# Performance work log

Hardware: AMD Instinct MI355X
Metric: run time of the kernel (lower is better)

The kernel has to match this reference:

```python
import jax, jax.numpy as jnp
import numpy as np
from math import factorial, sqrt

RS_IN = [(64, 0, 0), (64, 1, 0), (32, 2, 0)]
BATCH = 256


def _w3j(j1, j2, j3, m1, m2, m3):
    # Racah formula for the Wigner 3j symbol (integer l's)
    if m1 + m2 + m3 != 0 or not (abs(j1 - j2) <= j3 <= j1 + j2):
        return 0.0
    if abs(m1) > j1 or abs(m2) > j2 or abs(m3) > j3:
        return 0.0
    f = factorial
    pref = (-1.0) ** (j1 - j2 - m3) * sqrt(
        f(j1 + j2 - j3) * f(j1 - j2 + j3) * f(-j1 + j2 + j3) / f(j1 + j2 + j3 + 1)
        * f(j1 + m1) * f(j1 - m1) * f(j2 + m2) * f(j2 - m2) * f(j3 + m3) * f(j3 - m3))
    kmin = max(0, j2 - j3 - m1, j1 - j3 + m2)
    kmax = min(j1 + j2 - j3, j1 - m1, j2 + m2)
    s = 0.0
    for k in range(kmin, kmax + 1):
        s += (-1.0) ** k / (f(k) * f(j1 + j2 - j3 - k) * f(j1 - m1 - k)
                            * f(j2 + m2 - k) * f(j3 - j2 + m1 + k) * f(j3 - j1 - m2 + k))
    return pref * s


def _q(l):
    # unitary change of basis: complex spherical harmonics -> real basis
    q = np.zeros((2 * l + 1, 2 * l + 1), dtype=complex)
    q[l, l] = 1.0
    for m in range(1, l + 1):
        q[l + m, l + m] = (-1) ** m / sqrt(2)
        q[l + m, l - m] = 1 / sqrt(2)
        q[l - m, l - m] = 1j / sqrt(2)
        q[l - m, l + m] = -1j * (-1) ** m / sqrt(2)
    return q


def _real_w3j(la, lb, lc):
    # real-basis Wigner 3j tensor of shape (2la+1, 2lb+1, 2lc+1), Frobenius norm 1
    Cc = np.zeros((2 * la + 1, 2 * lb + 1, 2 * lc + 1))
    for ma in range(-la, la + 1):
        for mb in range(-lb, lb + 1):
            mc = -(ma + mb)
            if abs(mc) <= lc:
                Cc[la + ma, lb + mb, lc + mc] = _w3j(la, lb, lc, ma, mb, mc)
    T = np.einsum('im,jn,ko,mno->ijk', _q(la), _q(lb), _q(lc), Cc.astype(complex))
    idx = np.argmax(np.abs(T))
    T = T / (T.flat[idx] / abs(T.flat[idx]))  # fix global phase -> real tensor
    assert np.abs(T.imag).max() < 1e-6
    return np.real(T)


def _simplify(Rs):
    out = []
    for mul, l, p in Rs:
        if out and out[-1][1:] == (l, p):
            out[-1] = (out[-1][0] + mul, l, p)
        elif mul > 0:
            out.append((mul, l, p))
    return out


def _build(Rs_in):
    # Replicates e3nn tensor_square(Rs_in, sorted=True) with 'component' normalization,
    # producing the sparse mixing matrix as (row, col_i, col_j, value) with
    # col = col_i * dim_in + col_j  (never materialized densely).
    Rs = _simplify(Rs_in)
    dim_in = sum(m * (2 * l + 1) for m, l, _ in Rs)
    rows, ci, cj, vals, Rs_out = [], [], [], [], []
    index_out = 0
    index_1 = 0
    for a, (mul1, l1, p1) in enumerate(Rs):
        dim1 = mul1 * (2 * l1 + 1)
        # diagonal block: irrep with itself (sym/antisym multiplicity pairs)
        for lo in range(0, 2 * l1 + 1):
            w_all = np.arange(mul1 * mul1)
            u, v = w_all // mul1, w_all % mul1
            mask = (u <= v) if lo % 2 == 0 else (u < v)
            u, v = u[mask], v[mask]
            cnt = u.size
            if cnt == 0:
                continue
            C = _real_w3j(lo, l1, l1) * sqrt(2 * lo + 1)  # component norm
            k, i1, i2 = np.nonzero(C)
            cv = C[k, i1, i2]
            w = np.arange(cnt)
            rows.append((w[:, None] * (2 * lo + 1) + k[None, :]).ravel() + index_out)
            ci.append((u[:, None] * (2 * l1 + 1) + i1[None, :]).ravel() + index_1)
            cj.append((v[:, None] * (2 * l1 + 1) + i2[None, :]).ravel() + index_1)
            vals.append(np.tile(cv, cnt))
            Rs_out.append((cnt, lo, p1 * p1))
            index_out += cnt * (2 * lo + 1)
        index_2 = index_1 + dim1
        # off-diagonal blocks
        for (mul2, l2, p2) in Rs[a + 1:]:
            dim2 = mul2 * (2 * l2 + 1)
            for lo in range(abs(l1 - l2), l1 + l2 + 1):
                C = _real_w3j(lo, l1, l2) * sqrt(2 * lo + 1)
                k, i1, i2 = np.nonzero(C)
                cv = C[k, i1, i2]
                cnt = mul1 * mul2
                w = np.arange(cnt)
                u, v = w // mul2, w % mul2
                rows.append((w[:, None] * (2 * lo + 1) + k[None, :]).ravel() + index_out)
                ci.append((u[:, None] * (2 * l1 + 1) + i1[None, :]).ravel() + index_1)
                cj.append((v[:, None] * (2 * l2 + 1) + i2[None, :]).ravel() + index_2)
                vals.append(np.tile(cv, cnt))
                Rs_out.append((cnt, lo, p1 * p2))
                index_out += cnt * (2 * lo + 1)
            index_2 += dim2
        index_1 += dim1
    Rs_out = _simplify(Rs_out)
    # stable sort of output irreps by (l, p) -> row permutation (sorted=True)
    xs, j = [], 0
    for mul, l, p in Rs_out:
        d = mul * (2 * l + 1)
        xs.append((l, p, mul, j, d))
        j += d
    old2new = np.empty(j, dtype=np.int64)
    i = 0
    for l, p, mul, jj, d in sorted(xs):
        old2new[jj:jj + d] = np.arange(i, i + d)
        i += d
    rows = old2new[np.concatenate(rows)]
    return (rows.astype(np.int32), np.concatenate(ci).astype(np.int32),
            np.concatenate(cj).astype(np.int32),
            np.concatenate(vals).astype(np.float32), int(i), int(dim_in))


_ROWS, _COLI, _COLJ, _VALS, _DIM_OUT, _DIM_IN = _build(RS_IN)


def setup_inputs() -> dict:
    key = jax.random.key(0)
    features = jax.random.normal(key, (BATCH, _DIM_IN), dtype=jnp.float32)
    return {
        'features': features,
        'vals': jnp.asarray(_VALS),
        'rows': jnp.asarray(_ROWS),
        'col_i': jnp.asarray(_COLI),
        'col_j': jnp.asarray(_COLJ),
        'dim_out': _DIM_OUT,
    }


def reference(features, vals, rows, col_i, col_j, dim_out):
    # out[z, r] = sum_e vals[e] * f[z, col_i[e]] * f[z, col_j[e]]  scattered into rows[e]
    f = features.reshape(-1, features.shape[-1])              # (Z, dim_in)
    contrib = vals[None, :] * f[:, col_i] * f[:, col_j]       # (Z, nnz)
    out = jax.ops.segment_sum(contrib.T, rows, num_segments=dim_out)  # (dim_out, Z)
    return out.T.reshape(*features.shape[:-1], -1)
```

## Files before the change

### kernel.cpp

```cpp
#include <hip/hip_runtime.h>

#define BATCH 256
#define ZTILE 16
#define NZT 2
#define PADF 20
#define DIN_CAP 416

__global__ __launch_bounds__(256) void prep_t(
    const float* __restrict__ f, const int* __restrict__ rows,
    int* __restrict__ rstart, int* __restrict__ rend,
    float* __restrict__ fT, int nnz, int dim_in, int TB, int ctiles)
{
    const int bx = blockIdx.x;
    if (bx < TB) {
        __shared__ float lt[32][33];
        const int c0 = (bx % ctiles) * 32;
        const int z0 = (bx / ctiles) * 32;
        const int ic = threadIdx.x & 31;
        const int i0 = threadIdx.x >> 5;
#pragma unroll
        for (int k = 0; k < 4; ++k) {
            const int a = i0 + 8 * k;
            const int c = c0 + ic;
            lt[a][ic] = (c < dim_in) ? f[(size_t)(z0 + a) * dim_in + c] : 0.0f;
        }
        __syncthreads();
#pragma unroll
        for (int k = 0; k < 4; ++k) {
            const int b = i0 + 8 * k;
            const int c = c0 + b;
            if (c < dim_in)
                fT[(size_t)c * BATCH + z0 + ic] = lt[ic][b];
        }
    } else {
        const int e = (bx - TB) * 256 + threadIdx.x;
        if (e < nnz) {
            const int r = rows[e];
            if (e == 0 || rows[e - 1] != r) rstart[r] = e;
            if (e == nnz - 1 || rows[e + 1] != r) rend[r] = e + 1;
        }
    }
}

__device__ __forceinline__ void lds_sync()
{
    asm volatile("s_waitcnt lgkmcnt(0)" ::: "memory");
    __builtin_amdgcn_sched_barrier(0);
    __builtin_amdgcn_s_barrier();
    __builtin_amdgcn_sched_barrier(0);
}

__global__ __launch_bounds__(256) void tsq_main(
    const float* __restrict__ fT, const float* __restrict__ vals,
    const int* __restrict__ ci, const int* __restrict__ cj,
    const int* __restrict__ rstart, const int* __restrict__ rend,
    float* __restrict__ out, int dim_in, int dim_out, int nnz)
{
    __shared__ __align__(16) float fzT[DIN_CAP * PADF];

    const int r = blockIdx.x * blockDim.x + threadIdx.x;
    const bool valid = (r < dim_out);

    int s = 0, e1 = 0;
    if (valid) {
        const int ss = rstart[r];
        const int ee = rend[r];
        if (ss >= 0 && ee > ss && ee <= nnz) { s = ss; e1 = ee; }
    }

    const int zbase = blockIdx.y * (ZTILE * NZT);
    const int nchunk = dim_in * (ZTILE / 4);

    for (int t = 0; t < NZT; ++t) {
        const int z0 = zbase + t * ZTILE;

        for (int i = threadIdx.x; i < nchunk; i += blockDim.x) {
            const int c  = i >> 2;
            const int zq = i & 3;
            const float4 v = *(const float4*)(fT + (size_t)c * BATCH + z0 + zq * 4);
            *(float4*)(fzT + c * PADF + zq * 4) = v;
        }
        lds_sync();

        float4 a0 = {0,0,0,0}, a1 = {0,0,0,0}, a2 = {0,0,0,0}, a3 = {0,0,0,0};
        for (int e = s; e < e1; ++e) {
            const int   a = ci[e];
            const int   b = cj[e];
            const float v = vals[e];
            const float* ba = fzT + a * PADF;
            const float* bb = fzT + b * PADF;
            float4 xa, xb;
            xa = *(const float4*)(ba);      xb = *(const float4*)(bb);
            a0.x += v*xa.x*xb.x; a0.y += v*xa.y*xb.y; a0.z += v*xa.z*xb.z; a0.w += v*xa.w*xb.w;
            xa = *(const float4*)(ba + 4);  xb = *(const float4*)(bb + 4);
            a1.x += v*xa.x*xb.x; a1.y += v*xa.y*xb.y; a1.z += v*xa.z*xb.z; a1.w += v*xa.w*xb.w;
            xa = *(const float4*)(ba + 8);  xb = *(const float4*)(bb + 8);
            a2.x += v*xa.x*xb.x; a2.y += v*xa.y*xb.y; a2.z += v*xa.z*xb.z; a2.w += v*xa.w*xb.w;
            xa = *(const float4*)(ba + 12); xb = *(const float4*)(bb + 12);
            a3.x += v*xa.x*xb.x; a3.y += v*xa.y*xb.y; a3.z += v*xa.z*xb.z; a3.w += v*xa.w*xb.w;
        }

        if (valid) {
            float* o = out + (size_t)z0 * dim_out + r;
            const size_t d = dim_out;
            __builtin_nontemporal_store(a0.x, o);          __builtin_nontemporal_store(a0.y, o + d);
            __builtin_nontemporal_store(a0.z, o + 2*d);    __builtin_nontemporal_store(a0.w, o + 3*d);
            __builtin_nontemporal_store(a1.x, o + 4*d);    __builtin_nontemporal_store(a1.y, o + 5*d);
            __builtin_nontemporal_store(a1.z, o + 6*d);    __builtin_nontemporal_store(a1.w, o + 7*d);
            __builtin_nontemporal_store(a2.x, o + 8*d);    __builtin_nontemporal_store(a2.y, o + 9*d);
            __builtin_nontemporal_store(a2.z, o + 10*d);   __builtin_nontemporal_store(a2.w, o + 11*d);
            __builtin_nontemporal_store(a3.x, o + 12*d);   __builtin_nontemporal_store(a3.y, o + 13*d);
            __builtin_nontemporal_store(a3.z, o + 14*d);   __builtin_nontemporal_store(a3.w, o + 15*d);
        }
        lds_sync();
    }
}

__global__ __launch_bounds__(256) void tsq_fallback(
    const float* __restrict__ f, const float* __restrict__ vals,
    const int* __restrict__ ci, const int* __restrict__ cj,
    const int* __restrict__ rstart, const int* __restrict__ rend,
    float* __restrict__ out, int dim_in, int dim_out, int nnz)
{
    const int r = blockIdx.x * blockDim.x + threadIdx.x;
    if (r >= dim_out) return;
    const int z = blockIdx.y;
    const float* __restrict__ fb = f + (size_t)z * dim_in;
    const int ss = rstart[r];
    const int ee = rend[r];
    float acc = 0.0f;
    if (ss >= 0 && ee > ss && ee <= nnz) {
        for (int e = ss; e < ee; ++e)
            acc += vals[e] * fb[ci[e]] * fb[cj[e]];
    }
    out[(size_t)z * dim_out + r] = acc;
}

extern "C" void kernel_launch(void* const* d_in, const int* in_sizes, int n_in,
                              void* d_out, int out_size, void* d_ws, size_t ws_size,
                              hipStream_t stream)
{
    const float* f    = (const float*)d_in[0];
    const float* vals = (const float*)d_in[1];
    const int*   rows = (const int*)d_in[2];
    const int*   ci   = (const int*)d_in[3];
    const int*   cj   = (const int*)d_in[4];
    float*       out  = (float*)d_out;

    const int nnz     = in_sizes[1];
    const int nF      = in_sizes[0];
    const int dim_in  = nF / BATCH;
    const int dim_out = out_size / BATCH;

    int*   rstart = (int*)d_ws;
    int*   rend   = rstart + dim_out;
    float* fT     = (float*)(rend + dim_out);

    const int use_main = (dim_in <= DIN_CAP) &&
                         (ws_size >= (size_t)(2 * dim_out) * 4 + (size_t)nF * 4);

    const int ctiles = (dim_in + 31) / 32;
    const int TB = use_main ? ctiles * (BATCH / 32) : 0;
    const int NB = (nnz + 255) / 256;
    prep_t<<<TB + NB, 256, 0, stream>>>(f, rows, rstart, rend, fT,
                                        nnz, dim_in, TB, ctiles);

    if (use_main) {
        dim3 grid((dim_out + 255) / 256, BATCH / (ZTILE * NZT));
        tsq_main<<<grid, 256, 0, stream>>>(fT, vals, ci, cj, rstart, rend, out,
                                           dim_in, dim_out, nnz);
    } else {
        dim3 grid((dim_out + 255) / 256, BATCH);
        tsq_fallback<<<grid, 256, 0, stream>>>(f, vals, ci, cj, rstart, rend,
                                               out, dim_in, dim_out, nnz);
    }
}
```

Baseline: 35.79 us.

## Map output rows to waves with lanes over batch, staging output through LDS

Replaces the thread-per-row kernel that staged batch tiles of transposed features in LDS with a kernel where each wave handles eight output rows and each lane covers four batch entries, reading feature rows straight from the transposed global buffer. The results are collected in an LDS tile and then written out as row-coalesced stores. This removes the per-tile LDS fill and the barriers, and it removes divergence from rows with different nonzero counts, because all lanes in a wave share the same nonzero loop. The cost is that per-row work is serialized within a wave and feature reads now come from global memory or cache instead of LDS.

```diff
diff --git a/kernel.cpp b/kernel.cpp
--- a/kernel.cpp
+++ b/kernel.cpp
@@ -1,10 +1,11 @@
 #include <hip/hip_runtime.h>
 
 #define BATCH 256
-#define ZTILE 16
-#define NZT 2
-#define PADF 20
-#define DIN_CAP 416
+#define RPB 32
+#define RPW 8
+#define LSTR 260
+
+typedef float __attribute__((ext_vector_type(4))) fx4;
 
 __global__ __launch_bounds__(256) void prep_t(
     const float* __restrict__ f, const int* __restrict__ rows,
@@ -42,77 +43,56 @@
     }
 }
 
-__device__ __forceinline__ void lds_sync()
-{
-    asm volatile("s_waitcnt lgkmcnt(0)" ::: "memory");
-    __builtin_amdgcn_sched_barrier(0);
-    __builtin_amdgcn_s_barrier();
-    __builtin_amdgcn_sched_barrier(0);
-}
-
-__global__ __launch_bounds__(256) void tsq_main(
+__global__ __launch_bounds__(256) void tsq_rowwave(
     const float* __restrict__ fT, const float* __restrict__ vals,
     const int* __restrict__ ci, const int* __restrict__ cj,
     const int* __restrict__ rstart, const int* __restrict__ rend,
-    float* __restrict__ out, int dim_in, int dim_out, int nnz)
+    float* __restrict__ out, int dim_out, int nnz)
 {
-    __shared__ __align__(16) float fzT[DIN_CAP * PADF];
+    __shared__ __align__(16) float ot[RPB][LSTR];
 
-    const int r = blockIdx.x * blockDim.x + threadIdx.x;
-    const bool valid = (r < dim_out);
+    const int lane = threadIdx.x & 63;
+    const int wave = threadIdx.x >> 6;
+    const int r0   = blockIdx.x * RPB;
 
-    int s = 0, e1 = 0;
-    if (valid) {
-        const int ss = rstart[r];
-        const int ee = rend[r];
-        if (ss >= 0 && ee > ss && ee <= nnz) { s = ss; e1 = ee; }
+    for (int i = 0; i < RPW; ++i) {
+        const int rl = wave * RPW + i;
+        const int r  = r0 + rl;
+        fx4 acc = {0.f, 0.f, 0.f, 0.f};
+        if (r < dim_out) {
+            const int ss = rstart[r];
+            const int ee = rend[r];
+            if (ss >= 0 && ee > ss && ee <= nnz) {
+                for (int e = ss; e < ee; ++e) {
+                    const int   a = ci[e];
+                    const int   b = cj[e];
+                    const float v = vals[e];
+                    const fx4 xa = *(const fx4*)(fT + (size_t)a * BATCH + 4 * lane);
+                    const fx4 xb = *(const fx4*)(fT + (size_t)b * BATCH + 4 * lane);
+                    acc += v * xa * xb;
+                }
+            }
+        }
+        *(fx4*)(&ot[rl][4 * lane]) = acc;
     }
+    __syncthreads();
 
-    const int zbase = blockIdx.y * (ZTILE * NZT);
-    const int nchunk = dim_in * (ZTILE / 4);
-
-    for (int t = 0; t < NZT; ++t) {
-        const int z0 = zbase + t * ZTILE;
-
-        for (int i = threadIdx.x; i < nchunk; i += blockDim.x) {
-            const int c  = i >> 2;
-            const int zq = i & 3;
-            const float4 v = *(const float4*)(fT + (size_t)c * BATCH + z0 + zq * 4);
-            *(float4*)(fzT + c * PADF + zq * 4) = v;
+    const int rl   = threadIdx.x & 31;
+    const int qsel = threadIdx.x >> 5;
+    const int r    = r0 + rl;
+    if (r < dim_out) {
+        const size_t d = dim_out;
+#pragma unroll
+        for (int k = 0; k < 8; ++k) {
+            const int q = qsel + 8 * k;
+            const fx4 v = *(const fx4*)(&ot[rl][4 * q]);
+            const int z = 4 * q;
+            float* o = out + (size_t)z * d + r;
+            __builtin_nontemporal_store(v.x, o);
+            __builtin_nontemporal_store(v.y, o + d);
+            __builtin_nontemporal_store(v.z, o + 2 * d);
+            __builtin_nontemporal_store(v.w, o + 3 * d);
         }
-        lds_sync();
-
-        float4 a0 = {0,0,0,0}, a1 = {0,0,0,0}, a2 = {0,0,0,0}, a3 = {0,0,0,0};
-        for (int e = s; e < e1; ++e) {
-            const int   a = ci[e];
-            const int   b = cj[e];
-            const float v = vals[e];
-            const float* ba = fzT + a * PADF;
-            const float* bb = fzT + b * PADF;
-            float4 xa, xb;
-            xa = *(const float4*)(ba);      xb = *(const float4*)(bb);
-            a0.x += v*xa.x*xb.x; a0.y += v*xa.y*xb.y; a0.z += v*xa.z*xb.z; a0.w += v*xa.w*xb.w;
-            xa = *(const float4*)(ba + 4);  xb = *(const float4*)(bb + 4);
-            a1.x += v*xa.x*xb.x; a1.y += v*xa.y*xb.y; a1.z += v*xa.z*xb.z; a1.w += v*xa.w*xb.w;
-            xa = *(const float4*)(ba + 8);  xb = *(const float4*)(bb + 8);
-            a2.x += v*xa.x*xb.x; a2.y += v*xa.y*xb.y; a2.z += v*xa.z*xb.z; a2.w += v*xa.w*xb.w;
-            xa = *(const float4*)(ba + 12); xb = *(const float4*)(bb + 12);
-            a3.x += v*xa.x*xb.x; a3.y += v*xa.y*xb.y; a3.z += v*xa.z*xb.z; a3.w += v*xa.w*xb.w;
-        }
-
-        if (valid) {
-            float* o = out + (size_t)z0 * dim_out + r;
-            const size_t d = dim_out;
-            __builtin_nontemporal_store(a0.x, o);          __builtin_nontemporal_store(a0.y, o + d);
-            __builtin_nontemporal_store(a0.z, o + 2*d);    __builtin_nontemporal_store(a0.w, o + 3*d);
-            __builtin_nontemporal_store(a1.x, o + 4*d);    __builtin_nontemporal_store(a1.y, o + 5*d);
-            __builtin_nontemporal_store(a1.z, o + 6*d);    __builtin_nontemporal_store(a1.w, o + 7*d);
-            __builtin_nontemporal_store(a2.x, o + 8*d);    __builtin_nontemporal_store(a2.y, o + 9*d);
-            __builtin_nontemporal_store(a2.z, o + 10*d);   __builtin_nontemporal_store(a2.w, o + 11*d);
-            __builtin_nontemporal_store(a3.x, o + 12*d);   __builtin_nontemporal_store(a3.y, o + 13*d);
-            __builtin_nontemporal_store(a3.z, o + 14*d);   __builtin_nontemporal_store(a3.w, o + 15*d);
-        }
-        lds_sync();
     }
 }
 
@@ -156,7 +136,7 @@
     int*   rend   = rstart + dim_out;
     float* fT     = (float*)(rend + dim_out);
 
-    const int use_main = (dim_in <= DIN_CAP) &&
+    const int use_main = (nF == dim_in * BATCH) &&
                          (ws_size >= (size_t)(2 * dim_out) * 4 + (size_t)nF * 4);
 
     const int ctiles = (dim_in + 31) / 32;
@@ -166,9 +146,9 @@
                                         nnz, dim_in, TB, ctiles);
 
     if (use_main) {
-        dim3 grid((dim_out + 255) / 256, BATCH / (ZTILE * NZT));
-        tsq_main<<<grid, 256, 0, stream>>>(fT, vals, ci, cj, rstart, rend, out,
-                                           dim_in, dim_out, nnz);
+        const int nblk = (dim_out + RPB - 1) / RPB;
+        tsq_rowwave<<<nblk, 256, 0, stream>>>(fT, vals, ci, cj, rstart, rend,
+                                              out, dim_out, nnz);
     } else {
         dim3 grid((dim_out + 255) / 256, BATCH);
         tsq_fallback<<<grid, 256, 0, stream>>>(f, vals, ci, cj, rstart, rend,
```

Result: slower. 43.54 us (+21.6%).

## Double-buffer feature tiles in LDS and cache per-row indices in registers

Applied to the files above, without the earlier changes.

The main kernel now processes eight batch columns per tile instead of sixteen and loops over eight tiles per block. The next tile's global loads are staged in registers while the current tile is computed, then written into a second LDS buffer. The first four nonzeros of each row, with their indices pre-scaled to byte offsets, are held in registers so their ci, cj and vals loads are not repeated every tile. The grid shrinks to four batch groups, which means fewer blocks and less parallelism. In exchange it hides load latency and cuts per-tile index traffic. Rows with more than four nonzeros still reload from global memory.

```diff
diff --git a/kernel.cpp b/kernel.cpp
--- a/kernel.cpp
+++ b/kernel.cpp
@@ -1,9 +1,10 @@
 #include <hip/hip_runtime.h>
 
 #define BATCH 256
-#define ZTILE 16
-#define NZT 2
-#define PADF 20
+#define ZTILE 8
+#define TPB 8
+#define PADF 12
+#define CAP 4
 #define DIN_CAP 416
 
 __global__ __launch_bounds__(256) void prep_t(
@@ -50,15 +51,16 @@
     __builtin_amdgcn_sched_barrier(0);
 }
 
-__global__ __launch_bounds__(256) void tsq_main(
+__global__ __launch_bounds__(256) void tsq_pipe(
     const float* __restrict__ fT, const float* __restrict__ vals,
     const int* __restrict__ ci, const int* __restrict__ cj,
     const int* __restrict__ rstart, const int* __restrict__ rend,
     float* __restrict__ out, int dim_in, int dim_out, int nnz)
 {
-    __shared__ __align__(16) float fzT[DIN_CAP * PADF];
-
-    const int r = blockIdx.x * blockDim.x + threadIdx.x;
+    __shared__ __align__(16) float fz[2][DIN_CAP * PADF];
+
+    const int tid = threadIdx.x;
+    const int r   = blockIdx.x * 256 + tid;
     const bool valid = (r < dim_out);
 
     int s = 0, e1 = 0;
@@ -67,52 +69,108 @@
         const int ee = rend[r];
         if (ss >= 0 && ee > ss && ee <= nnz) { s = ss; e1 = ee; }
     }
-
-    const int zbase = blockIdx.y * (ZTILE * NZT);
+    const int cnt  = e1 - s;
+    const int creg = cnt < CAP ? cnt : CAP;
+
+    int pa_[CAP]; int pb_[CAP]; float pv_[CAP];
+#pragma unroll
+    for (int i = 0; i < CAP; ++i) {
+        if (i < creg) {
+            pa_[i] = ci[s + i] * (PADF * 4);
+            pb_[i] = cj[s + i] * (PADF * 4);
+            pv_[i] = vals[s + i];
+        } else { pa_[i] = 0; pb_[i] = 0; pv_[i] = 0.f; }
+    }
+
+    const int zbase  = blockIdx.y * (ZTILE * TPB);
     const int nchunk = dim_in * (ZTILE / 4);
 
-    for (int t = 0; t < NZT; ++t) {
+    float4 rg[4];
+    int    cc[4];
+#pragma unroll
+    for (int k = 0; k < 4; ++k) cc[k] = (tid + k * 256 < nchunk) ? tid + k * 256 : -1;
+
+#pragma unroll
+    for (int k = 0; k < 4; ++k) {
+        if (cc[k] >= 0) {
+            const int c  = cc[k] >> 1;
+            const int zq = cc[k] & 1;
+            rg[k] = *(const float4*)(fT + (size_t)c * BATCH + zbase + zq * 4);
+        }
+    }
+#pragma unroll
+    for (int k = 0; k < 4; ++k) {
+        if (cc[k] >= 0) {
+            const int c  = cc[k] >> 1;
+            const int zq = cc[k] & 1;
+            *(float4*)(&fz[0][c * PADF + zq * 4]) = rg[k];
+        }
+    }
+    lds_sync();
+
+    int cur = 0;
+    for (int t = 0; t < TPB; ++t) {
         const int z0 = zbase + t * ZTILE;
 
-        for (int i = threadIdx.x; i < nchunk; i += blockDim.x) {
-            const int c  = i >> 2;
-            const int zq = i & 3;
-            const float4 v = *(const float4*)(fT + (size_t)c * BATCH + z0 + zq * 4);
-            *(float4*)(fzT + c * PADF + zq * 4) = v;
-        }
-        lds_sync();
-
-        float4 a0 = {0,0,0,0}, a1 = {0,0,0,0}, a2 = {0,0,0,0}, a3 = {0,0,0,0};
-        for (int e = s; e < e1; ++e) {
-            const int   a = ci[e];
-            const int   b = cj[e];
-            const float v = vals[e];
-            const float* ba = fzT + a * PADF;
-            const float* bb = fzT + b * PADF;
+        if (t + 1 < TPB) {
+            const int zn = z0 + ZTILE;
+#pragma unroll
+            for (int k = 0; k < 4; ++k) {
+                if (cc[k] >= 0) {
+                    const int c  = cc[k] >> 1;
+                    const int zq = cc[k] & 1;
+                    rg[k] = *(const float4*)(fT + (size_t)c * BATCH + zn + zq * 4);
+                }
+            }
+        }
+
+        const char* fb = (const char*)fz[cur];
+        float4 a0 = {0,0,0,0}, a1 = {0,0,0,0};
+#pragma unroll
+        for (int i = 0; i < CAP; ++i) {
+            if (i < creg) {
+                const float v = pv_[i];
+                const char* ba = fb + pa_[i];
+                const char* bb = fb + pb_[i];
+                float4 xa, xb;
+                xa = *(const float4*)(ba);      xb = *(const float4*)(bb);
+                a0.x += v*xa.x*xb.x; a0.y += v*xa.y*xb.y; a0.z += v*xa.z*xb.z; a0.w += v*xa.w*xb.w;
+                xa = *(const float4*)(ba + 16); xb = *(const float4*)(bb + 16);
+                a1.x += v*xa.x*xb.x; a1.y += v*xa.y*xb.y; a1.z += v*xa.z*xb.z; a1.w += v*xa.w*xb.w;
+            }
+        }
+        for (int e = s + CAP; e < e1; ++e) {
+            const int a = ci[e], b = cj[e]; const float v = vals[e];
+            const char* ba = fb + a * (PADF * 4);
+            const char* bb = fb + b * (PADF * 4);
             float4 xa, xb;
             xa = *(const float4*)(ba);      xb = *(const float4*)(bb);
             a0.x += v*xa.x*xb.x; a0.y += v*xa.y*xb.y; a0.z += v*xa.z*xb.z; a0.w += v*xa.w*xb.w;
-            xa = *(const float4*)(ba + 4);  xb = *(const float4*)(bb + 4);
+            xa = *(const float4*)(ba + 16); xb = *(const float4*)(bb + 16);
             a1.x += v*xa.x*xb.x; a1.y += v*xa.y*xb.y; a1.z += v*xa.z*xb.z; a1.w += v*xa.w*xb.w;
-            xa = *(const float4*)(ba + 8);  xb = *(const float4*)(bb + 8);
-            a2.x += v*xa.x*xb.x; a2.y += v*xa.y*xb.y; a2.z += v*xa.z*xb.z; a2.w += v*xa.w*xb.w;
-            xa = *(const float4*)(ba + 12); xb = *(const float4*)(bb + 12);
-            a3.x += v*xa.x*xb.x; a3.y += v*xa.y*xb.y; a3.z += v*xa.z*xb.z; a3.w += v*xa.w*xb.w;
         }
 
         if (valid) {
             float* o = out + (size_t)z0 * dim_out + r;
             const size_t d = dim_out;
-            __builtin_nontemporal_store(a0.x, o);          __builtin_nontemporal_store(a0.y, o + d);
-            __builtin_nontemporal_store(a0.z, o + 2*d);    __builtin_nontemporal_store(a0.w, o + 3*d);
-            __builtin_nontemporal_store(a1.x, o + 4*d);    __builtin_nontemporal_store(a1.y, o + 5*d);
-            __builtin_nontemporal_store(a1.z, o + 6*d);    __builtin_nontemporal_store(a1.w, o + 7*d);
-            __builtin_nontemporal_store(a2.x, o + 8*d);    __builtin_nontemporal_store(a2.y, o + 9*d);
-            __builtin_nontemporal_store(a2.z, o + 10*d);   __builtin_nontemporal_store(a2.w, o + 11*d);
-            __builtin_nontemporal_store(a3.x, o + 12*d);   __builtin_nontemporal_store(a3.y, o + 13*d);
-            __builtin_nontemporal_store(a3.z, o + 14*d);   __builtin_nontemporal_store(a3.w, o + 15*d);
+            __builtin_nontemporal_store(a0.x, o);        __builtin_nontemporal_store(a0.y, o + d);
+            __builtin_nontemporal_store(a0.z, o + 2*d);  __builtin_nontemporal_store(a0.w, o + 3*d);
+            __builtin_nontemporal_store(a1.x, o + 4*d);  __builtin_nontemporal_store(a1.y, o + 5*d);
+            __builtin_nontemporal_store(a1.z, o + 6*d);  __builtin_nontemporal_store(a1.w, o + 7*d);
+        }
+
+        if (t + 1 < TPB) {
+#pragma unroll
+            for (int k = 0; k < 4; ++k) {
+                if (cc[k] >= 0) {
+                    const int c  = cc[k] >> 1;
+                    const int zq = cc[k] & 1;
+                    *(float4*)(&fz[cur ^ 1][c * PADF + zq * 4]) = rg[k];
+                }
+            }
         }
         lds_sync();
+        cur ^= 1;
     }
 }
 
@@ -166,8 +224,8 @@
                                         nnz, dim_in, TB, ctiles);
 
     if (use_main) {
-        dim3 grid((dim_out + 255) / 256, BATCH / (ZTILE * NZT));
-        tsq_main<<<grid, 256, 0, stream>>>(fT, vals, ci, cj, rstart, rend, out,
+        dim3 grid((dim_out + 255) / 256, BATCH / (ZTILE * TPB));
+        tsq_pipe<<<grid, 256, 0, stream>>>(fT, vals, ci, cj, rstart, rend, out,
                                            dim_in, dim_out, nnz);
     } else {
         dim3 grid((dim_out + 255) / 256, BATCH);
```

New measurement: 75.77 us. 2.12x slower.
